# Optimization experiments

Measured on AMD Instinct MI355X. Metric: run time of the kernel, lower is better.

Reference implementation:

```python
import jax, jax.numpy as jnp
import numpy as np

# Config constants (repo-level globals)
N, S, P = 4096, 64, 64          # total peds, scenes, peds per scene (uniform)
H, E, MLPD, BOT = 64, 16, 64, 32  # h_dim, EMBEDDING_DIM, MLP_DIM, BOTTLENECK_DIM
PRED_LEN = 12
MIN_DIM = 3                      # mlp_input_dim = [rel_pos(2), speed(1)]
PP_HID = 512                     # hidden width of mlp_pre_pool


def setup_inputs() -> dict:
    key = jax.random.key(0)
    ks = jax.random.split(key, 24)
    sc = 0.1
    starts = jnp.arange(S, dtype=jnp.int32) * P
    inp = {
        "last_pos": jax.random.normal(ks[0], (N, 2), jnp.float32),
        "last_pos_rel": jax.random.normal(ks[1], (N, 2), jnp.float32),
        "h0": jax.random.normal(ks[2], (1, N, H), jnp.float32),
        "c0": jax.random.normal(ks[3], (1, N, H), jnp.float32),
        "pred_ped_speed": jax.random.uniform(ks[4], (PRED_LEN, N, 1), jnp.float32),
        # spatial_embedding: Linear(3, E)
        "W_sp": jax.random.normal(ks[5], (MIN_DIM, E)) * sc, "b_sp": jnp.zeros(E),
        # LSTM cell (torch gate order i,f,g,o)
        "W_ih": jax.random.normal(ks[6], (E, 4 * H)) * sc, "b_ih": jnp.zeros(4 * H),
        "W_hh": jax.random.normal(ks[7], (H, 4 * H)) * sc, "b_hh": jnp.zeros(4 * H),
        # hidden2pos: Linear(H, 2)
        "W_h2p": jax.random.normal(ks[8], (H, 2)) * sc, "b_h2p": jnp.zeros(2),
        # pooling pos_embedding: Linear(3, E)
        "W_pe": jax.random.normal(ks[9], (MIN_DIM, E)) * sc, "b_pe": jnp.zeros(E),
        # mlp_pre_pool: [E+H, 512, BOT], relu, no BN
        "W_pp1": jax.random.normal(ks[10], (E + H, PP_HID)) * sc, "b_pp1": jnp.zeros(PP_HID),
        "W_pp2": jax.random.normal(ks[11], (PP_HID, BOT)) * sc, "b_pp2": jnp.zeros(BOT),
        # decoder mlp: [H+BOT, MLPD, H], relu, no BN
        "W_m1": jax.random.normal(ks[12], (H + BOT, MLPD)) * sc, "b_m1": jnp.zeros(MLPD),
        "W_m2": jax.random.normal(ks[13], (MLPD, H)) * sc, "b_m2": jnp.zeros(H),
        "seq_start_end": jnp.stack([starts, starts + P], axis=1),
        "train_or_test": 0,
    }
    return inp


def reference(last_pos, last_pos_rel, h0, c0, pred_ped_speed,
              W_sp, b_sp, W_ih, b_ih, W_hh, b_hh, W_h2p, b_h2p,
              W_pe, b_pe, W_pp1, b_pp1, W_pp2, b_pp2,
              W_m1, b_m1, W_m2, b_m2, seq_start_end, train_or_test):
    relu = jax.nn.relu

    def lstm_cell(x, h, c):
        g = x @ W_ih + b_ih + h @ W_hh + b_hh
        i, f, gg, o = jnp.split(g, 4, axis=-1)
        c = jax.nn.sigmoid(f) * c + jax.nn.sigmoid(i) * jnp.tanh(gg)
        h = jax.nn.sigmoid(o) * jnp.tanh(c)
        return h, c

    def pool(h, pos, spd):
        # uniform scenes: reshape [N,*] -> [S,P,*]; pairwise index [s,i,j]
        hg = h.reshape(S, P, H)
        pg = pos.reshape(S, P, 2)
        sg = spd.reshape(S, P, 1)
        # social feature [s,i,j] = pos[j] - pos[i]  (curr_end_pos_1 - curr_end_pos_2)
        rel = pg[:, None, :, :] - pg[:, :, None, :]              # [S,P,P,2]
        feat = jnp.concatenate(
            [rel, jnp.broadcast_to(sg[:, None, :, :], (S, P, P, 1))], -1)  # speed of j
        emb = feat @ W_pe + b_pe                                  # [S,P,P,E]
        pre = jnp.concatenate(
            [jnp.broadcast_to(hg[:, None, :, :], (S, P, P, H)), emb], -1)  # h of j
        x = relu(pre @ W_pp1 + b_pp1)
        x = relu(x @ W_pp2 + b_pp2)                               # [S,P,P,BOT]
        return x.max(axis=2).reshape(-1, BOT)                     # max over j -> [N,BOT]

    # speed used at step id is pred_ped_speed[id+1], last step reuses final speed
    spd_seq = jnp.concatenate([pred_ped_speed[1:], pred_ped_speed[-1:]], axis=0)
    x0 = jnp.concatenate([last_pos_rel, pred_ped_speed[0]], -1) @ W_sp + b_sp

    def step(carry, spd_t):
        h, c, lp, x = carry
        h, c = lstm_cell(x, h, c)
        rel_pos = h @ W_h2p + b_h2p
        curr = rel_pos + lp
        x_new = jnp.concatenate([rel_pos, spd_t], -1) @ W_sp + b_sp
        pool_h = pool(h, curr, spd_t)
        h_new = relu(relu(jnp.concatenate([h, pool_h], -1) @ W_m1 + b_m1) @ W_m2 + b_m2)
        return (h_new, c, curr, x_new), rel_pos

    carry = (h0[0], c0[0], last_pos, x0)
    _, rels = jax.lax.scan(step, carry, spd_seq)
    return rels  # [PRED_LEN, N, 2]
```

## Files before the change

kernel.cpp:

```cpp
#include <hip/hip_runtime.h>

typedef unsigned int  u32;
typedef unsigned short u16;
typedef float  f32x4 __attribute__((ext_vector_type(4)));
typedef u32    u32x4 __attribute__((ext_vector_type(4)));
typedef __bf16 bf16x8 __attribute__((ext_vector_type(8)));
typedef _Float16 f16;
typedef _Float16 f16x8 __attribute__((ext_vector_type(8)));
typedef _Float16 f16x2 __attribute__((ext_vector_type(2)));

static constexpr int NPED = 4096;
static constexpr int H = 64, E = 16, BOT = 32, PPH = 512;
static constexpr int TSTEPS = 12;

__device__ __forceinline__ float bf2f(u16 u) {
  return __builtin_bit_cast(float, ((u32)u) << 16);
}
__device__ __forceinline__ u16 f2bf(float f) {
  u32 u = __builtin_bit_cast(u32, f);
  u += 0x7fffu + ((u >> 16) & 1u);
  return (u16)(u >> 16);
}
__device__ __forceinline__ u16 f2h(float f) {
  return __builtin_bit_cast(u16, (f16)f);
}
__device__ __forceinline__ float sigm(float x) { return 1.f / (1.f + __expf(-x)); }
__device__ __forceinline__ float tanhf_(float x) {
  float t = fabsf(x);
  float e = __expf(-2.f * t);
  float r = (1.f - e) / (1.f + e);
  return x < 0.f ? -r : r;
}
__device__ __forceinline__ f16x8 relu8(f16x8 t) {
  const f16x8 z = {(f16)0, (f16)0, (f16)0, (f16)0, (f16)0, (f16)0, (f16)0, (f16)0};
#if __has_builtin(__builtin_elementwise_max)
  return __builtin_elementwise_max(t, z);
#else
  #pragma unroll
  for (int q = 0; q < 8; ++q) t[q] = t[q] > (f16)0 ? t[q] : (f16)0;
  return t;
#endif
}

static constexpr size_t OFF_C    = 0;
static constexpr size_t OFF_HL   = 1048576;
static constexpr size_t OFF_POS  = 2097152;
static constexpr size_t OFF_X    = 2129920;
static constexpr size_t OFF_POOL = 2392064;
static constexpr size_t OFF_ABF  = 2916352;
static constexpr size_t OFF_A3   = 7110656;
static constexpr size_t OFF_CST  = 7116800;
static constexpr size_t OFF_W2T  = 7118848;
static constexpr size_t OFF_GWH  = 7151616;
static constexpr size_t OFF_GWL  = 7200768;
static constexpr size_t OFF_D1H  = 7249920;
static constexpr size_t OFF_D1L  = 7262208;
static constexpr size_t OFF_D2H  = 7274496;
static constexpr size_t OFF_D2L  = 7282688;
static constexpr size_t OFF_PWH  = 7290880;
static constexpr size_t OFF_PWL  = 7356416;

static constexpr int POOL_SMEM = 64*520*2 + 32*520*2 + 16*512*2 + 16*4*2*16*4;

__global__ void k_setup(const float* __restrict__ last_pos, const float* __restrict__ last_pos_rel,
                        const float* __restrict__ c0, const float* __restrict__ pps,
                        const float* __restrict__ W_sp, const float* __restrict__ b_sp,
                        const float* __restrict__ W_pe, const float* __restrict__ b_pe,
                        const float* __restrict__ W_pp1, const float* __restrict__ b_pp1,
                        const float* __restrict__ W_pp2,
                        const float* __restrict__ W_ih, const float* __restrict__ W_hh,
                        const float* __restrict__ W_m1, const float* __restrict__ W_m2,
                        float* __restrict__ c, float* __restrict__ pos, float* __restrict__ x,
                        float* __restrict__ A3, float* __restrict__ Cst, u16* __restrict__ W2t,
                        u16* GWH, u16* GWL, u16* D1H, u16* D1L,
                        u16* D2H, u16* D2L, u16* PWH, u16* PWL)
{
  const int stride = gridDim.x * blockDim.x;
  const int tid0 = blockIdx.x * blockDim.x + threadIdx.x;
  for (int i = tid0; i < NPED * H; i += stride) c[i] = c0[i];
  for (int i = tid0; i < NPED * 2; i += stride) pos[i] = last_pos[i];
  for (int i = tid0; i < NPED * E; i += stride) {
    int n = i >> 4, e = i & 15;
    x[i] = last_pos_rel[2*n] * W_sp[e] + last_pos_rel[2*n+1] * W_sp[16+e]
         + pps[n] * W_sp[32+e] + b_sp[e];
  }
  for (int i = tid0; i < 3 * PPH; i += stride) {
    int r = i >> 9, k = i & 511;
    float s = 0.f;
    for (int e = 0; e < 16; ++e) s += W_pe[r*16+e] * W_pp1[(64+e)*PPH + k];
    A3[i] = s;
  }
  for (int i = tid0; i < PPH; i += stride) {
    float s = b_pp1[i];
    for (int e = 0; e < 16; ++e) s += b_pe[e] * W_pp1[(64+e)*PPH + i];
    Cst[i] = s;
  }
  for (int i = tid0; i < 32 * PPH; i += stride) {
    int n = i >> 9, k = i & 511;
    W2t[i] = f2h(W_pp2[k*32 + n]);
  }
  for (int i = tid0; i < 256*96; i += stride) {
    int n = i / 96, k = i - n*96;
    float wv = (k < 16) ? W_ih[k*256+n] : ((k < 80) ? W_hh[(k-16)*256+n] : 0.f);
    u16 hi = f2bf(wv); u16 lo = f2bf(wv - bf2f(hi));
    int idx = (((n>>4)*3 + (k>>5))*64 + ((k>>3)&3)*16 + (n&15))*8 + (k&7);
    GWH[idx] = hi; GWL[idx] = lo;
  }
  for (int i = tid0; i < 64*96; i += stride) {
    int n = i / 96, k = i - n*96;
    float wv = W_m1[k*64 + n];
    u16 hi = f2bf(wv); u16 lo = f2bf(wv - bf2f(hi));
    int idx = (((n>>4)*3 + (k>>5))*64 + ((k>>3)&3)*16 + (n&15))*8 + (k&7);
    D1H[idx] = hi; D1L[idx] = lo;
  }
  for (int i = tid0; i < 64*64; i += stride) {
    int n = i >> 6, k = i & 63;
    float wv = W_m2[k*64 + n];
    u16 hi = f2bf(wv); u16 lo = f2bf(wv - bf2f(hi));
    int idx = (((n>>4)*2 + (k>>5))*64 + ((k>>3)&3)*16 + (n&15))*8 + (k&7);
    D2H[idx] = hi; D2L[idx] = lo;
  }
  for (int i = tid0; i < 512*64; i += stride) {
    int n = i >> 6, k = i & 63;
    float wv = W_pp1[k*PPH + n];
    u16 hi = f2bf(wv); u16 lo = f2bf(wv - bf2f(hi));
    int idx = (((n>>4)*2 + (k>>5))*64 + ((k>>3)&3)*16 + (n&15))*8 + (k&7);
    PWH[idx] = hi; PWL[idx] = lo;
  }
}

template<int NT, int NKS>
__device__ __forceinline__ void mfma_block(
    const u16* __restrict__ WH, const u16* __restrict__ WL, int tile0, int lane,
    const float* arow, int acol0, f32x4* acc)
{
  u32x4 bh[NT][NKS], bl[NT][NKS];
  #pragma unroll
  for (int i = 0; i < NT; ++i)
    #pragma unroll
    for (int ks = 0; ks < NKS; ++ks) {
      int o = (((tile0 + i)*NKS + ks)*64 + lane)*8;
      bh[i][ks] = *(const u32x4*)(WH + o);
      bl[i][ks] = *(const u32x4*)(WL + o);
    }
  const int kg = lane >> 4;
  #pragma unroll
  for (int ks = 0; ks < NKS; ++ks) {
    f32x4 a0 = *(const f32x4*)(arow + acol0 + ks*32 + kg*8);
    f32x4 a1 = *(const f32x4*)(arow + acol0 + ks*32 + kg*8 + 4);
    float av[8] = {a0.x,a0.y,a0.z,a0.w,a1.x,a1.y,a1.z,a1.w};
    bf16x8 ah, al;
    #pragma unroll
    for (int j = 0; j < 8; ++j) {
      __bf16 hbits = (__bf16)av[j];
      ah[j] = hbits;
      al[j] = (__bf16)(av[j] - (float)hbits);
    }
    #pragma unroll
    for (int i = 0; i < NT; ++i) {
      bf16x8 BH = __builtin_bit_cast(bf16x8, bh[i][ks]);
      bf16x8 BL = __builtin_bit_cast(bf16x8, bl[i][ks]);
      acc[i] = __builtin_amdgcn_mfma_f32_16x16x32_bf16(ah, BH, acc[i], 0, 0, 0);
      acc[i] = __builtin_amdgcn_mfma_f32_16x16x32_bf16(ah, BL, acc[i], 0, 0, 0);
      acc[i] = __builtin_amdgcn_mfma_f32_16x16x32_bf16(al, BH, acc[i], 0, 0, 0);
    }
  }
}

__global__ __launch_bounds__(256) void k_step(
    int t,
    const float* __restrict__ h0, const float* __restrict__ pps,
    float* __restrict__ c, float* __restrict__ h_lstm,
    float* __restrict__ pos, float* __restrict__ x, const float* __restrict__ pool,
    const float* __restrict__ b_ih, const float* __restrict__ b_hh,
    const float* __restrict__ W_h2p, const float* __restrict__ b_h2p,
    const float* __restrict__ W_sp, const float* __restrict__ b_sp,
    const float* __restrict__ b_m1, const float* __restrict__ b_m2,
    const float* __restrict__ A3, const float* __restrict__ Cst,
    const u16* __restrict__ GWH, const u16* __restrict__ GWL,
    const u16* __restrict__ D1H, const u16* __restrict__ D1L,
    const u16* __restrict__ D2H, const u16* __restrict__ D2L,
    const u16* __restrict__ PWH, const u16* __restrict__ PWL,
    u16* __restrict__ a_bf, float* __restrict__ out)
{
  __shared__ float zin[16][100];
  __shared__ float o1[16][68];
  __shared__ float as_[16][100];
  __shared__ float hl[16][68];
  __shared__ float gl[16][260];
  __shared__ float rel_s[16][2], pos_s[16][2], spd_s[16];

  const int tid = threadIdx.x;
  const int p0 = blockIdx.x * 16;
  const int w = tid >> 6, lane = tid & 63, colq = lane & 15, kg = lane >> 4;
  const int tsp = (t + 1 < 12) ? t + 1 : 11;

  { int p = tid >> 4, e = tid & 15;
    as_[p][e] = x[(p0 + p) * E + e];
    as_[p][80 + e] = 0.f; }
  if (tid < 16) spd_s[tid] = pps[tsp * NPED + p0 + tid];
  if (t == 0) {
    #pragma unroll
    for (int q = 0; q < 4; ++q) {
      int idx = tid + 256*q; int p = idx >> 6, d = idx & 63;
      as_[p][16 + d] = h0[(p0 + p) * H + d];
    }
  } else {
    #pragma unroll
    for (int q = 0; q < 4; ++q) {
      int idx = tid + 256*q; int p = idx >> 6, d = idx & 63;
      zin[p][d] = h_lstm[(p0 + p) * H + d];
    }
    #pragma unroll
    for (int q = 0; q < 2; ++q) {
      int idx = tid + 256*q; int p = idx >> 5, d = idx & 31;
      zin[p][64 + d] = pool[(p0 + p) * BOT + d];
    }
  }
  __syncthreads();

  if (t > 0) {
    {
      f32x4 acc = {0.f, 0.f, 0.f, 0.f};
      mfma_block<1,3>(D1H, D1L, w, lane, &zin[colq][0], 0, &acc);
      int n = w*16 + colq;
      float bm = b_m1[n];
      #pragma unroll
      for (int r = 0; r < 4; ++r) o1[kg*4 + r][n] = fmaxf(acc[r] + bm, 0.f);
    }
    __syncthreads();
    {
      f32x4 acc = {0.f, 0.f, 0.f, 0.f};
      mfma_block<1,2>(D2H, D2L, w, lane, &o1[colq][0], 0, &acc);
      int n = w*16 + colq;
      float bm = b_m2[n];
      #pragma unroll
      for (int r = 0; r < 4; ++r) as_[kg*4 + r][16 + n] = fmaxf(acc[r] + bm, 0.f);
    }
    __syncthreads();
  }

  {
    f32x4 gacc[4];
    #pragma unroll
    for (int i = 0; i < 4; ++i) gacc[i] = (f32x4){0.f,0.f,0.f,0.f};
    mfma_block<2,3>(GWH, GWL, w*4,     lane, &as_[colq][0], 0, &gacc[0]);
    mfma_block<2,3>(GWH, GWL, w*4 + 2, lane, &as_[colq][0], 0, &gacc[2]);
    #pragma unroll
    for (int i = 0; i < 4; ++i) {
      int n = (w*4 + i)*16 + colq;
      float bb = b_ih[n] + b_hh[n];
      #pragma unroll
      for (int r = 0; r < 4; ++r) gl[kg*4 + r][n] = gacc[i][r] + bb;
    }
  }
  __syncthreads();

  #pragma unroll
  for (int q = 0; q < 4; ++q) {
    int idx = tid + 256*q; int p = idx >> 6, d = idx & 63; int n = p0 + p;
    float gi = gl[p][d], gf = gl[p][64 + d], gg = gl[p][128 + d], go = gl[p][192 + d];
    float cv = c[n*H + d];
    float cn = sigm(gf) * cv + sigm(gi) * tanhf_(gg);
    float hv = sigm(go) * tanhf_(cn);
    c[n*H + d] = cn;
    hl[p][d] = hv;
    h_lstm[n*H + d] = hv;
  }
  __syncthreads();

  {
    int p = tid >> 4, l = tid & 15;
    f32x4 hv = *(const f32x4*)(&hl[p][0] + l*4);
    float s0 = hv.x * W_h2p[(l*4+0)*2]   + hv.y * W_h2p[(l*4+1)*2]
             + hv.z * W_h2p[(l*4+2)*2]   + hv.w * W_h2p[(l*4+3)*2];
    float s1 = hv.x * W_h2p[(l*4+0)*2+1] + hv.y * W_h2p[(l*4+1)*2+1]
             + hv.z * W_h2p[(l*4+2)*2+1] + hv.w * W_h2p[(l*4+3)*2+1];
    #pragma unroll
    for (int m = 1; m < 16; m <<= 1) {
      s0 += __shfl_xor(s0, m, 64);
      s1 += __shfl_xor(s1, m, 64);
    }
    if (l == 0) {
      float r0 = s0 + b_h2p[0], r1 = s1 + b_h2p[1];
      int n = p0 + p;
      float px = pos[n*2] + r0, py = pos[n*2+1] + r1;
      pos[n*2] = px; pos[n*2+1] = py;
      rel_s[p][0] = r0; rel_s[p][1] = r1;
      pos_s[p][0] = px; pos_s[p][1] = py;
      out[(t*NPED + n)*2] = r0; out[(t*NPED + n)*2 + 1] = r1;
    }
  }
  __syncthreads();

  if (t < 11) {
    {
      int p = tid >> 4, e = tid & 15;
      float xv = rel_s[p][0] * W_sp[e] + rel_s[p][1] * W_sp[16+e]
               + spd_s[p] * W_sp[32+e] + b_sp[e];
      x[(p0 + p) * E + e] = xv;
    }
    {
      f32x4 pacc[8];
      #pragma unroll
      for (int i = 0; i < 8; ++i) pacc[i] = (f32x4){0.f,0.f,0.f,0.f};
      mfma_block<4,2>(PWH, PWL, w*8,     lane, &hl[colq][0], 0, &pacc[0]);
      mfma_block<4,2>(PWH, PWL, w*8 + 4, lane, &hl[colq][0], 0, &pacc[4]);
      #pragma unroll
      for (int i = 0; i < 8; ++i) {
        int n = (w*8 + i)*16 + colq;
        float a3x = A3[n], a3y = A3[512 + n], a3s = A3[1024 + n], cst = Cst[n];
        #pragma unroll
        for (int r = 0; r < 4; ++r) {
          int p2 = kg*4 + r;
          float val = pacc[i][r] + pos_s[p2][0]*a3x + pos_s[p2][1]*a3y
                    + spd_s[p2]*a3s + cst;
          a_bf[(size_t)(p0 + p2)*PPH + n] = f2h(val);
        }
      }
    }
  }
}

__global__ __launch_bounds__(1024) void k_pool(
    const u16* __restrict__ a_bf, const float* __restrict__ pos,
    const float* __restrict__ A3, const u16* __restrict__ W2t,
    const float* __restrict__ b_pp2, float* __restrict__ pool)
{
  constexpr int LDA = 520;
  extern __shared__ char smem_raw[];
  u16* a_s  = (u16*)smem_raw;
  u16* w2_s = a_s + 64 * LDA;
  f16* v_s  = (f16*)(w2_s + 32 * LDA);
  float* red = (float*)(v_s + 16 * 512);

  const int tid = threadIdx.x;
  const int s = blockIdx.y;
  const int i0 = blockIdx.x * 16;

  for (int idx = tid; idx < 4096; idx += 1024) {
    int r = idx >> 6, c8 = (idx & 63) * 8;
    *(u32x4*)&a_s[r * LDA + c8] = *(const u32x4*)&a_bf[(s * 64 + r) * PPH + c8];
  }
  for (int idx = tid; idx < 2048; idx += 1024) {
    int r = idx >> 6, c8 = (idx & 63) * 8;
    *(u32x4*)&w2_s[r * LDA + c8] = *(const u32x4*)&W2t[r * PPH + c8];
  }
  for (int idx = tid; idx < 4096; idx += 1024) {
    int i = idx >> 8, k2 = (idx & 255) * 2;
    int n = s * 64 + i0 + i;
    float px = pos[n * 2], py = pos[n * 2 + 1];
    float v0 = px * A3[k2]     + py * A3[512 + k2];
    float v1 = px * A3[k2 + 1] + py * A3[512 + k2 + 1];
    f16x2 pk = { (f16)v0, (f16)v1 };
    *(f16x2*)&v_s[i * 512 + k2] = pk;
  }
  __syncthreads();

  const int lane = tid & 63, w = tid >> 6;
  const int jq = w & 3, g = w >> 2;
  const int col = lane & 15, kg = lane >> 4;
  const int aoff  = (jq * 16 + col) * LDA + kg * 8;
  const int w0off = col * LDA + kg * 8;
  const int w1off = (col + 16) * LDA + kg * 8;
  const float b20 = b_pp2[col];
  const float b21 = b_pp2[col + 16];
  const f32x4 vzero = {0.f, 0.f, 0.f, 0.f};

  f32x4 accA[4], accB[4];
  #pragma unroll
  for (int ii = 0; ii < 4; ++ii) { accA[ii] = vzero; accB[ii] = vzero; }

  for (int kk = 0; kk < 16; ++kk) {
    const int ke = kk * 32;
    f16x8 a8  = __builtin_bit_cast(f16x8, *(const u32x4*)&a_s[aoff + ke]);
    f16x8 bw0 = __builtin_bit_cast(f16x8, *(const u32x4*)&w2_s[w0off + ke]);
    f16x8 bw1 = __builtin_bit_cast(f16x8, *(const u32x4*)&w2_s[w1off + ke]);
    #pragma unroll
    for (int ii = 0; ii < 4; ++ii) {
      f16x8 v8 = *(const f16x8*)&v_s[(g * 4 + ii) * 512 + ke + kg * 8];
      f16x8 tq = relu8(a8 - v8);
      accA[ii] = __builtin_amdgcn_mfma_f32_16x16x32_f16(tq, bw0, accA[ii], 0, 0, 0);
      accB[ii] = __builtin_amdgcn_mfma_f32_16x16x32_f16(tq, bw1, accB[ii], 0, 0, 0);
    }
  }

  #pragma unroll
  for (int ii = 0; ii < 4; ++ii) {
    float m0 = 0.f, m1 = 0.f;
    #pragma unroll
    for (int r = 0; r < 4; ++r) {
      m0 = fmaxf(m0, accA[ii][r] + b20);
      m1 = fmaxf(m1, accB[ii][r] + b21);
    }
    m0 = fmaxf(m0, __shfl_xor(m0, 16, 64));
    m0 = fmaxf(m0, __shfl_xor(m0, 32, 64));
    m1 = fmaxf(m1, __shfl_xor(m1, 16, 64));
    m1 = fmaxf(m1, __shfl_xor(m1, 32, 64));
    if (kg == 0) {
      red[((w * 4 + ii) * 2 + 0) * 16 + col] = m0;
      red[((w * 4 + ii) * 2 + 1) * 16 + col] = m1;
    }
  }
  __syncthreads();

  if (tid < 512) {
    int gg = tid >> 7, ii = (tid >> 5) & 3, tile = (tid >> 4) & 1, cc = tid & 15;
    float m = red[(((gg * 4 + 0) * 4 + ii) * 2 + tile) * 16 + cc];
    #pragma unroll
    for (int q = 1; q < 4; ++q)
      m = fmaxf(m, red[(((gg * 4 + q) * 4 + ii) * 2 + tile) * 16 + cc]);
    int i = i0 + gg * 4 + ii;
    pool[(s * 64 + i) * 32 + tile * 16 + cc] = m;
  }
}

extern "C" void kernel_launch(void* const* d_in, const int* in_sizes, int n_in,
                              void* d_out, int out_size, void* d_ws, size_t ws_size,
                              hipStream_t stream)
{
  const float* last_pos     = (const float*)d_in[0];
  const float* last_pos_rel = (const float*)d_in[1];
  const float* h0    = (const float*)d_in[2];
  const float* c0    = (const float*)d_in[3];
  const float* pps   = (const float*)d_in[4];
  const float* W_sp  = (const float*)d_in[5];
  const float* b_sp  = (const float*)d_in[6];
  const float* W_ih  = (const float*)d_in[7];
  const float* b_ih  = (const float*)d_in[8];
  const float* W_hh  = (const float*)d_in[9];
  const float* b_hh  = (const float*)d_in[10];
  const float* W_h2p = (const float*)d_in[11];
  const float* b_h2p = (const float*)d_in[12];
  const float* W_pe  = (const float*)d_in[13];
  const float* b_pe  = (const float*)d_in[14];
  const float* W_pp1 = (const float*)d_in[15];
  const float* b_pp1 = (const float*)d_in[16];
  const float* W_pp2 = (const float*)d_in[17];
  const float* b_pp2 = (const float*)d_in[18];
  const float* W_m1  = (const float*)d_in[19];
  const float* b_m1  = (const float*)d_in[20];
  const float* W_m2  = (const float*)d_in[21];
  const float* b_m2  = (const float*)d_in[22];

  char* ws = (char*)d_ws;
  float* c_buf  = (float*)(ws + OFF_C);
  float* h_lstm = (float*)(ws + OFF_HL);
  float* pos    = (float*)(ws + OFF_POS);
  float* x_buf  = (float*)(ws + OFF_X);
  float* pool   = (float*)(ws + OFF_POOL);
  u16*   a_bf   = (u16*)(ws + OFF_ABF);
  float* A3     = (float*)(ws + OFF_A3);
  float* Cst    = (float*)(ws + OFF_CST);
  u16*   W2t    = (u16*)(ws + OFF_W2T);
  u16* GWH = (u16*)(ws + OFF_GWH); u16* GWL = (u16*)(ws + OFF_GWL);
  u16* D1H = (u16*)(ws + OFF_D1H); u16* D1L = (u16*)(ws + OFF_D1L);
  u16* D2H = (u16*)(ws + OFF_D2H); u16* D2L = (u16*)(ws + OFF_D2L);
  u16* PWH = (u16*)(ws + OFF_PWH); u16* PWL = (u16*)(ws + OFF_PWL);
  float* out    = (float*)d_out;

  hipFuncSetAttribute(reinterpret_cast<const void*>(k_pool),
                      hipFuncAttributeMaxDynamicSharedMemorySize, POOL_SMEM);

  k_setup<<<512, 256, 0, stream>>>(last_pos, last_pos_rel, c0, pps, W_sp, b_sp,
                                   W_pe, b_pe, W_pp1, b_pp1, W_pp2,
                                   W_ih, W_hh, W_m1, W_m2,
                                   c_buf, pos, x_buf, A3, Cst, W2t,
                                   GWH, GWL, D1H, D1L, D2H, D2L, PWH, PWL);
  for (int t = 0; t < TSTEPS; ++t) {
    k_step<<<256, 256, 0, stream>>>(t, h0, pps, c_buf, h_lstm, pos, x_buf, pool,
                                    b_ih, b_hh, W_h2p, b_h2p, W_sp, b_sp,
                                    b_m1, b_m2, A3, Cst,
                                    GWH, GWL, D1H, D1L, D2H, D2L, PWH, PWL,
                                    a_bf, out);
    if (t < TSTEPS - 1)
      k_pool<<<dim3(4, 64), 1024, POOL_SMEM, stream>>>(a_bf, pos, A3, W2t, b_pp2, pool);
  }
}
```

Measured before the change: 318.0 us.

## Fuse pooling and LSTM step into one kernel with double-buffered activations

Merges the per-step pool kernel and step kernel into one k_fused kernel per timestep. Each block pools its 16 pedestrians, then runs the decoder MLP, LSTM, position update and next-step pre-pool projection in shared memory. The pool output stays in shared memory, which removes the global round trip for pool and h and about 11 kernel launches. Because other blocks of the same scene still read the previous step's activation buffer, the buffer is double-buffered in extra workspace. A fallback to the old path is kept if the workspace is too small. The 1024-thread blocks do the small MLP and LSTM with mostly idle warps, which may lower throughput on that part.

```diff
diff --git a/kernel.cpp b/kernel.cpp
--- a/kernel.cpp
+++ b/kernel.cpp
@@ -59,8 +59,12 @@
 static constexpr size_t OFF_D2L  = 7282688;
 static constexpr size_t OFF_PWH  = 7290880;
 static constexpr size_t OFF_PWL  = 7356416;
+static constexpr size_t OFF_ABF2 = 7421952;
+static constexpr size_t ABF_BYTES = (size_t)NPED * PPH * 2;
+static constexpr size_t WS_NEED_FUSED = OFF_ABF2 + ABF_BYTES;
 
 static constexpr int POOL_SMEM = 64*520*2 + 32*520*2 + 16*512*2 + 16*4*2*16*4;
+static constexpr int FUSED_SMEM = POOL_SMEM + 16*32*4 + 64 + 128 + 128;
 
 __global__ void k_setup(const float* __restrict__ last_pos, const float* __restrict__ last_pos_rel,
                         const float* __restrict__ c0, const float* __restrict__ pps,
@@ -130,11 +134,10 @@
 }
 
 template<int NT, int NKS>
-__device__ __forceinline__ void mfma_block(
-    const u16* __restrict__ WH, const u16* __restrict__ WL, int tile0, int lane,
-    const float* arow, int acol0, f32x4* acc)
+__device__ __forceinline__ void load_frags(const u16* __restrict__ WH, const u16* __restrict__ WL,
+                                           int tile0, int lane,
+                                           u32x4 (&bh)[NT][NKS], u32x4 (&bl)[NT][NKS])
 {
-  u32x4 bh[NT][NKS], bl[NT][NKS];
   #pragma unroll
   for (int i = 0; i < NT; ++i)
     #pragma unroll
@@ -143,11 +146,17 @@
       bh[i][ks] = *(const u32x4*)(WH + o);
       bl[i][ks] = *(const u32x4*)(WL + o);
     }
+}
+
+template<int NT, int NKS>
+__device__ __forceinline__ void mfma_compute(const u32x4 (&bh)[NT][NKS], const u32x4 (&bl)[NT][NKS],
+                                             int lane, const float* arow, f32x4* acc)
+{
   const int kg = lane >> 4;
   #pragma unroll
   for (int ks = 0; ks < NKS; ++ks) {
-    f32x4 a0 = *(const f32x4*)(arow + acol0 + ks*32 + kg*8);
-    f32x4 a1 = *(const f32x4*)(arow + acol0 + ks*32 + kg*8 + 4);
+    f32x4 a0 = *(const f32x4*)(arow + ks*32 + kg*8);
+    f32x4 a1 = *(const f32x4*)(arow + ks*32 + kg*8 + 4);
     float av[8] = {a0.x,a0.y,a0.z,a0.w,a1.x,a1.y,a1.z,a1.w};
     bf16x8 ah, al;
     #pragma unroll
@@ -165,6 +174,16 @@
       acc[i] = __builtin_amdgcn_mfma_f32_16x16x32_bf16(al, BH, acc[i], 0, 0, 0);
     }
   }
+}
+
+template<int NT, int NKS>
+__device__ __forceinline__ void mfma_block(
+    const u16* __restrict__ WH, const u16* __restrict__ WL, int tile0, int lane,
+    const float* arow, int acol0, f32x4* acc)
+{
+  u32x4 bh[NT][NKS], bl[NT][NKS];
+  load_frags<NT,NKS>(WH, WL, tile0, lane, bh, bl);
+  mfma_compute<NT,NKS>(bh, bl, lane, arow + acol0, acc);
 }
 
 __global__ __launch_bounds__(256) void k_step(
@@ -412,6 +431,237 @@
       m = fmaxf(m, red[(((gg * 4 + q) * 4 + ii) * 2 + tile) * 16 + cc]);
     int i = i0 + gg * 4 + ii;
     pool[(s * 64 + i) * 32 + tile * 16 + cc] = m;
+  }
+}
+
+__global__ __launch_bounds__(1024) void k_fused(
+    int t,
+    const float* __restrict__ pps,
+    float* __restrict__ c, float* __restrict__ h_lstm,
+    float* __restrict__ pos, float* __restrict__ x,
+    const float* __restrict__ b_ih, const float* __restrict__ b_hh,
+    const float* __restrict__ W_h2p, const float* __restrict__ b_h2p,
+    const float* __restrict__ W_sp, const float* __restrict__ b_sp,
+    const float* __restrict__ b_m1, const float* __restrict__ b_m2,
+    const float* __restrict__ A3, const float* __restrict__ Cst,
+    const u16* __restrict__ GWH, const u16* __restrict__ GWL,
+    const u16* __restrict__ D1H, const u16* __restrict__ D1L,
+    const u16* __restrict__ D2H, const u16* __restrict__ D2L,
+    const u16* __restrict__ PWH, const u16* __restrict__ PWL,
+    const u16* __restrict__ W2t, const float* __restrict__ b_pp2,
+    const u16* __restrict__ a_read, u16* __restrict__ a_write,
+    float* __restrict__ out)
+{
+  constexpr int LDA = 520;
+  extern __shared__ char smem_raw[];
+  u16*   a_s    = (u16*)smem_raw;
+  u16*   w2_s   = a_s + 64 * LDA;
+  f16*   v_s    = (f16*)(w2_s + 32 * LDA);
+  float* red    = (float*)(v_s + 16 * 512);
+  float* pool_s = red + 16*4*2*16;
+  float* spd_s  = pool_s + 16*32;
+  float* rel_s  = spd_s + 16;
+  float* pos_s  = rel_s + 32;
+  float* zin = (float*)smem_raw;
+  float* o1  = zin + 16*100;
+  float* as_ = o1  + 16*68;
+  float* hl  = as_ + 16*100;
+  float* gl  = hl  + 16*68;
+
+  const int tid = threadIdx.x;
+  const int s = blockIdx.y;
+  const int i0 = blockIdx.x * 16;
+  const int p0 = s * 64 + i0;
+  const int lane = tid & 63, w = tid >> 6;
+  const int colq = lane & 15, kg = lane >> 4;
+  const int tsp = (t + 1 < 12) ? t + 1 : 11;
+
+  float hreg = h_lstm[(p0 + (tid >> 6)) * H + (tid & 63)];
+  float xreg = 0.f;
+  if (tid < 256) xreg = x[(p0 + (tid >> 4)) * E + (tid & 15)];
+  if (tid < 16) spd_s[tid] = pps[tsp * NPED + p0 + tid];
+
+  for (int idx = tid; idx < 4096; idx += 1024) {
+    int r = idx >> 6, c8 = (idx & 63) * 8;
+    *(u32x4*)&a_s[r * LDA + c8] = *(const u32x4*)&a_read[(s * 64 + r) * PPH + c8];
+  }
+  for (int idx = tid; idx < 2048; idx += 1024) {
+    int r = idx >> 6, c8 = (idx & 63) * 8;
+    *(u32x4*)&w2_s[r * LDA + c8] = *(const u32x4*)&W2t[r * PPH + c8];
+  }
+  for (int idx = tid; idx < 4096; idx += 1024) {
+    int i = idx >> 8, k2 = (idx & 255) * 2;
+    int n = s * 64 + i0 + i;
+    float px = pos[n * 2], py = pos[n * 2 + 1];
+    float v0 = px * A3[k2]     + py * A3[512 + k2];
+    float v1 = px * A3[k2 + 1] + py * A3[512 + k2 + 1];
+    f16x2 pk = { (f16)v0, (f16)v1 };
+    *(f16x2*)&v_s[i * 512 + k2] = pk;
+  }
+  __syncthreads();
+
+  {
+    const int jq = w & 3, g = w >> 2;
+    const int aoff  = (jq * 16 + colq) * LDA + kg * 8;
+    const int w0off = colq * LDA + kg * 8;
+    const int w1off = (colq + 16) * LDA + kg * 8;
+    const float b20 = b_pp2[colq];
+    const float b21 = b_pp2[colq + 16];
+    const f32x4 vzero = {0.f, 0.f, 0.f, 0.f};
+
+    f32x4 accA[4], accB[4];
+    #pragma unroll
+    for (int ii = 0; ii < 4; ++ii) { accA[ii] = vzero; accB[ii] = vzero; }
+
+    for (int kk = 0; kk < 16; ++kk) {
+      const int ke = kk * 32;
+      f16x8 a8  = __builtin_bit_cast(f16x8, *(const u32x4*)&a_s[aoff + ke]);
+      f16x8 bw0 = __builtin_bit_cast(f16x8, *(const u32x4*)&w2_s[w0off + ke]);
+      f16x8 bw1 = __builtin_bit_cast(f16x8, *(const u32x4*)&w2_s[w1off + ke]);
+      #pragma unroll
+      for (int ii = 0; ii < 4; ++ii) {
+        f16x8 v8 = *(const f16x8*)&v_s[(g * 4 + ii) * 512 + ke + kg * 8];
+        f16x8 tq = relu8(a8 - v8);
+        accA[ii] = __builtin_amdgcn_mfma_f32_16x16x32_f16(tq, bw0, accA[ii], 0, 0, 0);
+        accB[ii] = __builtin_amdgcn_mfma_f32_16x16x32_f16(tq, bw1, accB[ii], 0, 0, 0);
+      }
+    }
+
+    #pragma unroll
+    for (int ii = 0; ii < 4; ++ii) {
+      float m0 = 0.f, m1 = 0.f;
+      #pragma unroll
+      for (int r = 0; r < 4; ++r) {
+        m0 = fmaxf(m0, accA[ii][r] + b20);
+        m1 = fmaxf(m1, accB[ii][r] + b21);
+      }
+      m0 = fmaxf(m0, __shfl_xor(m0, 16, 64));
+      m0 = fmaxf(m0, __shfl_xor(m0, 32, 64));
+      m1 = fmaxf(m1, __shfl_xor(m1, 16, 64));
+      m1 = fmaxf(m1, __shfl_xor(m1, 32, 64));
+      if (kg == 0) {
+        red[((w * 4 + ii) * 2 + 0) * 16 + colq] = m0;
+        red[((w * 4 + ii) * 2 + 1) * 16 + colq] = m1;
+      }
+    }
+  }
+  __syncthreads();
+
+  if (tid < 512) {
+    int gg = tid >> 7, ii = (tid >> 5) & 3, tile = (tid >> 4) & 1, cc = tid & 15;
+    float m = red[(((gg * 4 + 0) * 4 + ii) * 2 + tile) * 16 + cc];
+    #pragma unroll
+    for (int q = 1; q < 4; ++q)
+      m = fmaxf(m, red[(((gg * 4 + q) * 4 + ii) * 2 + tile) * 16 + cc]);
+    pool_s[(gg * 4 + ii) * 32 + tile * 16 + cc] = m;
+  }
+  __syncthreads();
+
+  { int p = tid >> 6, d = tid & 63; zin[p * 100 + d] = hreg; }
+  if (tid < 512) { int p = tid >> 5, dd = tid & 31; zin[p * 100 + 64 + dd] = pool_s[p * 32 + dd]; }
+  if (tid < 256) { int p = tid >> 4, e = tid & 15;
+                   as_[p * 100 + e] = xreg; as_[p * 100 + 80 + e] = 0.f; }
+  u32x4 gh[1][3], glo[1][3];
+  load_frags<1,3>(GWH, GWL, w, lane, gh, glo);
+  __syncthreads();
+
+  if (w < 4) {
+    f32x4 acc = {0.f, 0.f, 0.f, 0.f};
+    u32x4 dh[1][3], dl[1][3];
+    load_frags<1,3>(D1H, D1L, w, lane, dh, dl);
+    mfma_compute<1,3>(dh, dl, lane, &zin[colq * 100], &acc);
+    int n = w * 16 + colq;
+    float bm = b_m1[n];
+    #pragma unroll
+    for (int r = 0; r < 4; ++r) o1[(kg * 4 + r) * 68 + n] = fmaxf(acc[r] + bm, 0.f);
+  }
+  __syncthreads();
+
+  if (w < 4) {
+    f32x4 acc = {0.f, 0.f, 0.f, 0.f};
+    u32x4 dh[1][2], dl[1][2];
+    load_frags<1,2>(D2H, D2L, w, lane, dh, dl);
+    mfma_compute<1,2>(dh, dl, lane, &o1[colq * 68], &acc);
+    int n = w * 16 + colq;
+    float bm = b_m2[n];
+    #pragma unroll
+    for (int r = 0; r < 4; ++r) as_[(kg * 4 + r) * 100 + 16 + n] = fmaxf(acc[r] + bm, 0.f);
+  }
+  __syncthreads();
+
+  {
+    f32x4 acc = {0.f, 0.f, 0.f, 0.f};
+    mfma_compute<1,3>(gh, glo, lane, &as_[colq * 100], &acc);
+    int n = w * 16 + colq;
+    float bb = b_ih[n] + b_hh[n];
+    #pragma unroll
+    for (int r = 0; r < 4; ++r) gl[(kg * 4 + r) * 260 + n] = acc[r] + bb;
+  }
+  u32x4 ph[2][2], pl[2][2];
+  if (t < 11) load_frags<2,2>(PWH, PWL, w * 2, lane, ph, pl);
+  __syncthreads();
+
+  { int p = tid >> 6, d = tid & 63; int n = p0 + p;
+    float gi = gl[p*260 + d], gf = gl[p*260 + 64 + d],
+          gg = gl[p*260 + 128 + d], go = gl[p*260 + 192 + d];
+    float cv = c[n*H + d];
+    float cn = sigm(gf) * cv + sigm(gi) * tanhf_(gg);
+    float hv = sigm(go) * tanhf_(cn);
+    c[n*H + d] = cn;
+    hl[p*68 + d] = hv;
+    h_lstm[n*H + d] = hv;
+  }
+  __syncthreads();
+
+  if (tid < 256) {
+    int p = tid >> 4, l = tid & 15;
+    f32x4 hv = *(const f32x4*)(&hl[p * 68] + l * 4);
+    float s0 = hv.x * W_h2p[(l*4+0)*2]   + hv.y * W_h2p[(l*4+1)*2]
+             + hv.z * W_h2p[(l*4+2)*2]   + hv.w * W_h2p[(l*4+3)*2];
+    float s1 = hv.x * W_h2p[(l*4+0)*2+1] + hv.y * W_h2p[(l*4+1)*2+1]
+             + hv.z * W_h2p[(l*4+2)*2+1] + hv.w * W_h2p[(l*4+3)*2+1];
+    #pragma unroll
+    for (int m = 1; m < 16; m <<= 1) {
+      s0 += __shfl_xor(s0, m, 64);
+      s1 += __shfl_xor(s1, m, 64);
+    }
+    if (l == 0) {
+      float r0 = s0 + b_h2p[0], r1 = s1 + b_h2p[1];
+      int n = p0 + p;
+      float px = pos[n*2] + r0, py = pos[n*2+1] + r1;
+      pos[n*2] = px; pos[n*2+1] = py;
+      rel_s[p*2+0] = r0; rel_s[p*2+1] = r1;
+      pos_s[p*2+0] = px; pos_s[p*2+1] = py;
+      out[(t*NPED + n)*2] = r0; out[(t*NPED + n)*2 + 1] = r1;
+    }
+  }
+  __syncthreads();
+
+  if (t < 11) {
+    if (tid < 256) {
+      int p = tid >> 4, e = tid & 15;
+      float xv = rel_s[p*2+0] * W_sp[e] + rel_s[p*2+1] * W_sp[16+e]
+               + spd_s[p] * W_sp[32+e] + b_sp[e];
+      x[(p0 + p) * E + e] = xv;
+    }
+    {
+      f32x4 pacc[2];
+      pacc[0] = (f32x4){0.f,0.f,0.f,0.f};
+      pacc[1] = (f32x4){0.f,0.f,0.f,0.f};
+      mfma_compute<2,2>(ph, pl, lane, &hl[colq * 68], pacc);
+      #pragma unroll
+      for (int i = 0; i < 2; ++i) {
+        int n = (w * 2 + i) * 16 + colq;
+        float a3x = A3[n], a3y = A3[512 + n], a3s = A3[1024 + n], cst = Cst[n];
+        #pragma unroll
+        for (int r = 0; r < 4; ++r) {
+          int p2 = kg * 4 + r;
+          float val = pacc[i][r] + pos_s[p2*2+0]*a3x + pos_s[p2*2+1]*a3y
+                    + spd_s[p2]*a3s + cst;
+          a_write[(size_t)(p0 + p2) * PPH + n] = f2h(val);
+        }
+      }
+    }
   }
 }
 
@@ -449,7 +699,7 @@
   float* pos    = (float*)(ws + OFF_POS);
   float* x_buf  = (float*)(ws + OFF_X);
   float* pool   = (float*)(ws + OFF_POOL);
-  u16*   a_bf   = (u16*)(ws + OFF_ABF);
+  u16*   abuf0  = (u16*)(ws + OFF_ABF);
   float* A3     = (float*)(ws + OFF_A3);
   float* Cst    = (float*)(ws + OFF_CST);
   u16*   W2t    = (u16*)(ws + OFF_W2T);
@@ -457,23 +707,46 @@
   u16* D1H = (u16*)(ws + OFF_D1H); u16* D1L = (u16*)(ws + OFF_D1L);
   u16* D2H = (u16*)(ws + OFF_D2H); u16* D2L = (u16*)(ws + OFF_D2L);
   u16* PWH = (u16*)(ws + OFF_PWH); u16* PWL = (u16*)(ws + OFF_PWL);
+  u16*   abuf1  = (u16*)(ws + OFF_ABF2);
   float* out    = (float*)d_out;
+
+  const bool fused_ok = (ws_size >= WS_NEED_FUSED);
 
   hipFuncSetAttribute(reinterpret_cast<const void*>(k_pool),
                       hipFuncAttributeMaxDynamicSharedMemorySize, POOL_SMEM);
+  hipFuncSetAttribute(reinterpret_cast<const void*>(k_fused),
+                      hipFuncAttributeMaxDynamicSharedMemorySize, FUSED_SMEM);
 
   k_setup<<<512, 256, 0, stream>>>(last_pos, last_pos_rel, c0, pps, W_sp, b_sp,
                                    W_pe, b_pe, W_pp1, b_pp1, W_pp2,
                                    W_ih, W_hh, W_m1, W_m2,
                                    c_buf, pos, x_buf, A3, Cst, W2t,
                                    GWH, GWL, D1H, D1L, D2H, D2L, PWH, PWL);
-  for (int t = 0; t < TSTEPS; ++t) {
-    k_step<<<256, 256, 0, stream>>>(t, h0, pps, c_buf, h_lstm, pos, x_buf, pool,
-                                    b_ih, b_hh, W_h2p, b_h2p, W_sp, b_sp,
-                                    b_m1, b_m2, A3, Cst,
-                                    GWH, GWL, D1H, D1L, D2H, D2L, PWH, PWL,
-                                    a_bf, out);
-    if (t < TSTEPS - 1)
-      k_pool<<<dim3(4, 64), 1024, POOL_SMEM, stream>>>(a_bf, pos, A3, W2t, b_pp2, pool);
-  }
-}
+
+  k_step<<<256, 256, 0, stream>>>(0, h0, pps, c_buf, h_lstm, pos, x_buf, pool,
+                                  b_ih, b_hh, W_h2p, b_h2p, W_sp, b_sp,
+                                  b_m1, b_m2, A3, Cst,
+                                  GWH, GWL, D1H, D1L, D2H, D2L, PWH, PWL,
+                                  abuf0, out);
+
+  if (fused_ok) {
+    for (int t = 1; t < TSTEPS; ++t) {
+      const u16* ar = ((t - 1) & 1) ? abuf1 : abuf0;
+      u16*       aw = (t & 1)       ? abuf1 : abuf0;
+      k_fused<<<dim3(4, 64), 1024, FUSED_SMEM, stream>>>(
+          t, pps, c_buf, h_lstm, pos, x_buf,
+          b_ih, b_hh, W_h2p, b_h2p, W_sp, b_sp, b_m1, b_m2, A3, Cst,
+          GWH, GWL, D1H, D1L, D2H, D2L, PWH, PWL,
+          W2t, b_pp2, ar, aw, out);
+    }
+  } else {
+    for (int t = 1; t < TSTEPS; ++t) {
+      k_pool<<<dim3(4, 64), 1024, POOL_SMEM, stream>>>(abuf0, pos, A3, W2t, b_pp2, pool);
+      k_step<<<256, 256, 0, stream>>>(t, h0, pps, c_buf, h_lstm, pos, x_buf, pool,
+                                      b_ih, b_hh, W_h2p, b_h2p, W_sp, b_sp,
+                                      b_m1, b_m2, A3, Cst,
+                                      GWH, GWL, D1H, D1L, D2H, D2L, PWH, PWL,
+                                      abuf0, out);
+    }
+  }
+}
```

Result: faster. 288.0 us (-9.4%).
